# Kernel optimization log

Hardware: AMD Instinct MI355X
Metric: run time of the kernel (lower is better)

Reference implementation:

```python
import jax, jax.numpy as jnp
import numpy as np

# VoxelGrid constants (create_empty not shown in source; fixed to a realistic dense grid)
W, L, H = 64, 64, 64
VOXEL_SIZE = 0.05
ORIGIN = 0.0  # per-axis origin, same for all batches
ROUNDING_OFFSET = 0.5
MIN_POINTS_PER_VOXEL = 10


def setup_inputs() -> dict:
    key = jax.random.key(0)
    k1, k2 = jax.random.split(key)
    B, C, N = 4, 32, 200_000
    extent = W * VOXEL_SIZE  # 3.2
    # uniform coords slightly extending past the grid so a few points are OOB
    point_coordinates = jax.random.uniform(
        k1, (B, 3, N), jnp.float32, minval=-0.02, maxval=extent + 0.02)
    point_attributes = jax.random.normal(k2, (B, C, N), jnp.float32)
    return {"point_coordinates": point_coordinates,
            "point_attributes": point_attributes}


def reference(point_coordinates, point_attributes):
    B, C, N = point_attributes.shape
    V = W * L * H
    bounds = jnp.array([W, L, H], jnp.int32)

    # point -> integer voxel coordinates (origin = 0)
    coords = jnp.floor((point_coordinates - ORIGIN) / VOXEL_SIZE
                       + ROUNDING_OFFSET).astype(jnp.int32)      # [B,3,N]
    in_bounds = jnp.all((coords >= 0) & (coords < bounds[None, :, None]),
                        axis=1)                                   # [B,N]
    flat = coords[:, 0] * (L * H) + coords[:, 1] * H + coords[:, 2]
    # route OOB points to segment V which is dropped by segment ops
    flat = jnp.where(in_bounds, flat, V)                          # [B,N]

    def per_batch(idx, attrs, mask):
        # idx [N] int32, attrs [C,N], mask [N] bool
        counts = jax.ops.segment_sum(mask.astype(jnp.int32), idx,
                                     num_segments=V)              # [V]
        vals = jnp.where(mask[None, :], attrs, -jnp.inf)          # [C,N]
        pooled = jax.ops.segment_max(vals.T, idx, num_segments=V).T  # [C,V]
        pooled = jnp.where(counts[None, :] > 0, pooled, jnp.zeros_like(pooled))
        occ = (counts >= MIN_POINTS_PER_VOXEL).astype(attrs.dtype)   # [V]
        return pooled, occ

    data, occ = jax.vmap(per_batch)(flat, point_attributes, in_bounds)
    voxeldata = data.reshape(B, C, W, L, H)
    voxeloccupancy = occ.reshape(B, 1, W, L, H)
    return voxeldata, voxeloccupancy
```

## Files before the change

### kernel.cpp

```cpp
#include <hip/hip_runtime.h>
#include <math.h>


#define GW 64
#define GL 64
#define GH 64
#define GV (GW * GL * GH)
#define NB 4
#define MIN_PTS 10

__device__ __forceinline__ int bin_coord(float x) {
    float m = __fmul_rn(x, 20.0f);
    float r = __fadd_rn(m, 0.5f);
    return (int)floorf(r);
}

__global__ void zero_kernel(uint4* __restrict__ p, int n4) {
    int i = blockIdx.x * blockDim.x + threadIdx.x;
    if (i < n4) p[i] = make_uint4(0u, 0u, 0u, 0u);
}

__global__ void hist_transpose_kernel(const float* __restrict__ coords,
                                      const float* __restrict__ attrs,
                                      int* __restrict__ counts,
                                      int* __restrict__ vox,
                                      int* __restrict__ rank,
                                      float* __restrict__ attrsT,
                                      size_t strideT,
                                      int b0, int N) {
    __shared__ float lds[4][64 * 33];
    int t = threadIdx.x;
    int w = t >> 6;
    int l = t & 63;
    int n = blockIdx.x * 256 + t;
    int b = b0 + blockIdx.y;

    if (n < N) {
        const float* pc = coords + (size_t)b * 3 * N;
        int ix = bin_coord(pc[n]);
        int iy = bin_coord(pc[n + N]);
        int iz = bin_coord(pc[n + 2 * N]);
        bool ok = (unsigned)ix < (unsigned)GW && (unsigned)iy < (unsigned)GL &&
                  (unsigned)iz < (unsigned)GH;
        int v = ok ? ((ix << 12) | (iy << 6) | iz) : -1;
        vox[(size_t)b * N + n] = v;
        if (ok) rank[(size_t)b * N + n] = atomicAdd(&counts[b * GV + v], 1);

        const float* pa = attrs + (size_t)b * 32 * N + n;
        float* row = &lds[w][l * 33];
#pragma unroll
        for (int c = 0; c < 32; ++c)
            row[c] = pa[(size_t)c * N];
    }
    __syncthreads();

    float* dbase = attrsT + (size_t)blockIdx.y * strideT;
    int wbase = blockIdx.x * 256 + w * 64;
    int j = l & 7;
#pragma unroll
    for (int s = 0; s < 8; ++s) {
        int q = s * 8 + (l >> 3);
        int p = wbase + q;
        if (p < N) {
            const float* src = &lds[w][q * 33 + j * 4];
            float4 val = make_float4(src[0], src[1], src[2], src[3]);
            *(float4*)&dbase[(size_t)p * 32 + j * 4] = val;
        }
    }
}

__global__ void hist_kernel(const float* __restrict__ coords,
                            int* __restrict__ counts,
                            int* __restrict__ vox,
                            int* __restrict__ rank,
                            int N) {
    int n = blockIdx.x * blockDim.x + threadIdx.x;
    int b = blockIdx.y;
    if (n >= N) return;
    const float* pc = coords + (size_t)b * 3 * N;
    int ix = bin_coord(pc[n]);
    int iy = bin_coord(pc[n + N]);
    int iz = bin_coord(pc[n + 2 * N]);
    bool ok = (unsigned)ix < (unsigned)GW && (unsigned)iy < (unsigned)GL &&
              (unsigned)iz < (unsigned)GH;
    int v = ok ? ((ix << 12) | (iy << 6) | iz) : -1;
    vox[(size_t)b * N + n] = v;
    if (ok) rank[(size_t)b * N + n] = atomicAdd(&counts[b * GV + v], 1);
}

__global__ void transpose_kernel(const float* __restrict__ attrs,
                                 float* __restrict__ attrsT,
                                 size_t strideT, int b0, int N) {
    __shared__ float lds[4][64 * 33];
    int t = threadIdx.x;
    int w = t >> 6;
    int l = t & 63;
    int n = blockIdx.x * 256 + t;
    int b = b0 + blockIdx.y;
    if (n < N) {
        const float* pa = attrs + (size_t)b * 32 * N + n;
        float* row = &lds[w][l * 33];
#pragma unroll
        for (int c = 0; c < 32; ++c)
            row[c] = pa[(size_t)c * N];
    }
    __syncthreads();
    float* dbase = attrsT + (size_t)blockIdx.y * strideT;
    int wbase = blockIdx.x * 256 + w * 64;
    int j = l & 7;
#pragma unroll
    for (int s = 0; s < 8; ++s) {
        int q = s * 8 + (l >> 3);
        int p = wbase + q;
        if (p < N) {
            const float* src = &lds[w][q * 33 + j * 4];
            float4 val = make_float4(src[0], src[1], src[2], src[3]);
            *(float4*)&dbase[(size_t)p * 32 + j * 4] = val;
        }
    }
}

__global__ void scan_blocks_kernel(const int* __restrict__ counts,
                                   int* __restrict__ offsets,
                                   int* __restrict__ blocksums) {
    __shared__ int lds[256];
    int t = threadIdx.x;
    int base = blockIdx.x * 1024 + t * 4;
    int4 c = *(const int4*)&counts[base];
    int s0 = c.x, s1 = s0 + c.y, s2 = s1 + c.z, s3 = s2 + c.w;
    lds[t] = s3;
    __syncthreads();
    for (int d = 1; d < 256; d <<= 1) {
        int v = (t >= d) ? lds[t - d] : 0;
        __syncthreads();
        if (t >= d) lds[t] += v;
        __syncthreads();
    }
    int excl = (t > 0) ? lds[t - 1] : 0;
    int4 o;
    o.x = excl; o.y = excl + s0; o.z = excl + s1; o.w = excl + s2;
    *(int4*)&offsets[base] = o;
    if (t == 255) blocksums[blockIdx.x] = lds[255];
}

__global__ void scan_sums_kernel(int* __restrict__ blocksums) {
    __shared__ int lds[256];
    int t = threadIdx.x;
    int4 c = *(const int4*)&blocksums[t * 4];
    int s0 = c.x, s1 = s0 + c.y, s2 = s1 + c.z, s3 = s2 + c.w;
    lds[t] = s3;
    __syncthreads();
    for (int d = 1; d < 256; d <<= 1) {
        int v = (t >= d) ? lds[t - d] : 0;
        __syncthreads();
        if (t >= d) lds[t] += v;
        __syncthreads();
    }
    int excl = (t > 0) ? lds[t - 1] : 0;
    int4 o;
    o.x = excl; o.y = excl + s0; o.z = excl + s1; o.w = excl + s2;
    *(int4*)&blocksums[t * 4] = o;
}

__global__ void scan_add_kernel(int* __restrict__ offsets,
                                const int* __restrict__ blocksums) {
    int i = blockIdx.x * blockDim.x + threadIdx.x;
    int s = blocksums[(i * 4) >> 10];
    int4 o = *(int4*)&offsets[i * 4];
    o.x += s; o.y += s; o.z += s; o.w += s;
    *(int4*)&offsets[i * 4] = o;
}

__global__ void scatter_idx_kernel(const int* __restrict__ vox,
                                   const int* __restrict__ rank,
                                   const int* __restrict__ offsets,
                                   int* __restrict__ sorted_idx,
                                   int N) {
    int n = blockIdx.x * blockDim.x + threadIdx.x;
    int b = blockIdx.y;
    if (n >= N) return;
    int v = vox[(size_t)b * N + n];
    if (v < 0) return;
    sorted_idx[offsets[b * GV + v] + rank[(size_t)b * N + n]] = n;
}

__global__ void segmax3_kernel(const float* __restrict__ attrsT,
                               const int* __restrict__ counts,
                               const int* __restrict__ offsets,
                               const int* __restrict__ sorted_idx,
                               float* __restrict__ vdata,
                               float* __restrict__ occ,
                               size_t strideT,
                               int b0) {
    __shared__ float acc[64 * 33];
    __shared__ int cnt_l[64];
    __shared__ int off_l[64];
    int t = threadIdx.x;
    int w = t >> 6;
    int lane = t & 63;
    int g = lane >> 5;
    int c = lane & 31;
    int b = b0 + blockIdx.y;
    int v0 = blockIdx.x * 64;

    if (t < 64) {
        int bv = b * GV + v0 + t;
        cnt_l[t] = counts[bv];
        off_l[t] = offsets[bv];
    }
    __syncthreads();

    const float* sbase = attrsT + (size_t)blockIdx.y * strideT;
#pragma unroll
    for (int pp = 0; pp < 8; ++pp) {
        int vl = w * 16 + pp * 2 + g;
        int cnt = cnt_l[vl];
        int off = off_l[vl];
        float m = -INFINITY;
        for (int k = 0; k < cnt; ++k) {
            int idx = sorted_idx[off + k];
            m = fmaxf(m, sbase[(size_t)idx * 32 + c]);
        }
        acc[vl * 33 + c] = (cnt > 0) ? m : 0.0f;
    }
    __syncthreads();

    int vv = v0 + lane;
#pragma unroll
    for (int cc = 0; cc < 8; ++cc) {
        int ch = cc * 4 + w;
        vdata[(((size_t)(b * 32 + ch)) << 18) + vv] = acc[lane * 33 + ch];
    }
    if (t < 64)
        occ[b * GV + v0 + t] = (cnt_l[t] >= MIN_PTS) ? 1.0f : 0.0f;
}

__global__ void segmax_kernel(const float* __restrict__ attrs,
                              const int* __restrict__ counts,
                              const int* __restrict__ offsets,
                              const int* __restrict__ sorted_idx,
                              float* __restrict__ vdata,
                              float* __restrict__ occ,
                              int N) {
    int t = blockIdx.x * blockDim.x + threadIdx.x;
    int v = t & (GV - 1);
    int c = (t >> 18) & 31;
    int b = t >> 23;
    int bv = (b << 18) | v;
    int cnt = counts[bv];
    int off = offsets[bv];
    const float* row = attrs + ((size_t)(b * 32 + c)) * N;
    float m = -INFINITY;
    for (int k = 0; k < cnt; ++k) {
        m = fmaxf(m, row[sorted_idx[off + k]]);
    }
    vdata[((size_t)(b * 32 + c) << 18) | v] = (cnt > 0) ? m : 0.0f;
    if (c == 0) occ[bv] = (cnt >= MIN_PTS) ? 1.0f : 0.0f;
}

__device__ __forceinline__ unsigned enc_f32(float f) {
    unsigned u = __float_as_uint(f);
    return (u & 0x80000000u) ? ~u : (u | 0x80000000u);
}
__device__ __forceinline__ float dec_f32(unsigned u) {
    return (u & 0x80000000u) ? __uint_as_float(u & 0x7FFFFFFFu)
                             : __uint_as_float(~u);
}

__global__ void init_kernel(uint4* __restrict__ data4, uint4* __restrict__ cnt4,
                            int nData4, int nCnt4) {
    int i = blockIdx.x * blockDim.x + threadIdx.x;
    uint4 z = make_uint4(0u, 0u, 0u, 0u);
    if (i < nData4) data4[i] = z;
    else if (i < nData4 + nCnt4) cnt4[i - nData4] = z;
}

__global__ void scatter_kernel(const float* __restrict__ coords,
                               const float* __restrict__ attrs,
                               unsigned* __restrict__ bits,
                               int* __restrict__ counts,
                               int N, int C) {
    int n = blockIdx.x * blockDim.x + threadIdx.x;
    int b = blockIdx.y;
    if (n >= N) return;
    const float* pc = coords + (size_t)b * 3 * N;
    int ix = bin_coord(pc[n]);
    int iy = bin_coord(pc[n + N]);
    int iz = bin_coord(pc[n + 2 * N]);
    if ((unsigned)ix >= (unsigned)GW || (unsigned)iy >= (unsigned)GL ||
        (unsigned)iz >= (unsigned)GH)
        return;
    int v = (ix << 12) | (iy << 6) | iz;
    atomicAdd(&counts[b * GV + v], 1);
    const float* pa = attrs + (size_t)b * C * N + n;
    unsigned* pb = bits + (size_t)b * C * GV + v;
    for (int c = 0; c < C; ++c)
        atomicMax(&pb[(size_t)c * GV], enc_f32(pa[(size_t)c * N]));
}

__global__ void finalize_kernel(unsigned* __restrict__ data,
                                const int* __restrict__ counts,
                                float* __restrict__ occ, int C) {
    int i = blockIdx.x * blockDim.x + threadIdx.x;
    int nData4 = NB * C * GV / 4;
    int nOcc4 = NB * GV / 4;
    if (i < nData4) {
        int idx = i << 2;
        int v = idx & (GV - 1);
        int b = idx / (C * GV);
        int4 cv = *(const int4*)&counts[b * GV + v];
        uint4 u = *(const uint4*)&data[idx];
        float4 r;
        r.x = cv.x > 0 ? dec_f32(u.x) : 0.0f;
        r.y = cv.y > 0 ? dec_f32(u.y) : 0.0f;
        r.z = cv.z > 0 ? dec_f32(u.z) : 0.0f;
        r.w = cv.w > 0 ? dec_f32(u.w) : 0.0f;
        *(float4*)&data[idx] = r;
    } else if (i < nData4 + nOcc4) {
        int j = (i - nData4) << 2;
        int4 cv = *(const int4*)&counts[j];
        float4 r;
        r.x = cv.x >= MIN_PTS ? 1.0f : 0.0f;
        r.y = cv.y >= MIN_PTS ? 1.0f : 0.0f;
        r.z = cv.z >= MIN_PTS ? 1.0f : 0.0f;
        r.w = cv.w >= MIN_PTS ? 1.0f : 0.0f;
        *(float4*)&occ[j] = r;
    }
}

extern "C" void kernel_launch(void* const* d_in, const int* in_sizes, int n_in,
                              void* d_out, int out_size, void* d_ws, size_t ws_size,
                              hipStream_t stream) {
    const float* coords = (const float*)d_in[0];
    const float* attrs  = (const float*)d_in[1];
    int N = in_sizes[0] / (NB * 3);
    int C = in_sizes[1] / (NB * N);

    size_t wsCommon = (size_t)(2 * NB * GV + 4096 + 3 * NB * N) * 4;
    size_t oneT  = (size_t)N * 32 * 4;
    size_t fullT = (size_t)NB * N * 32 * 4;

    if (C == 32 && ws_size >= wsCommon + oneT) {
        int* counts     = (int*)d_ws;
        int* offsets    = counts + (size_t)NB * GV;
        int* blocksums  = offsets + (size_t)NB * GV;
        int* vox        = blocksums + 4096;
        int* rank       = vox + (size_t)NB * N;
        int* sorted_idx = rank + (size_t)NB * N;
        float* attrsT   = (float*)(sorted_idx + (size_t)NB * N);
        float* vdata    = (float*)d_out;
        float* occ      = (float*)d_out + (size_t)NB * 32 * GV;

        int nCnt4 = NB * GV / 4;
        zero_kernel<<<(nCnt4 + 255) / 256, 256, 0, stream>>>((uint4*)counts,
                                                             nCnt4);
        dim3 pgrid((N + 255) / 256, NB);
        bool full = (ws_size >= wsCommon + fullT);

        if (full) {
            hist_transpose_kernel<<<pgrid, 256, 0, stream>>>(
                coords, attrs, counts, vox, rank, attrsT, (size_t)N * 32, 0, N);
        } else {
            hist_kernel<<<pgrid, 256, 0, stream>>>(coords, counts, vox, rank,
                                                   N);
        }

        scan_blocks_kernel<<<NB * GV / 1024, 256, 0, stream>>>(counts, offsets,
                                                               blocksums);
        scan_sums_kernel<<<1, 256, 0, stream>>>(blocksums);
        scan_add_kernel<<<NB * GV / 1024, 256, 0, stream>>>(offsets, blocksums);

        scatter_idx_kernel<<<pgrid, 256, 0, stream>>>(vox, rank, offsets,
                                                      sorted_idx, N);

        if (full) {
            segmax3_kernel<<<dim3(GV / 64, NB), 256, 0, stream>>>(
                attrsT, counts, offsets, sorted_idx, vdata, occ,
                (size_t)N * 32, 0);
        } else {
            for (int b = 0; b < NB; ++b) {
                transpose_kernel<<<dim3((N + 255) / 256, 1), 256, 0, stream>>>(
                    attrs, attrsT, 0, b, N);
                segmax3_kernel<<<dim3(GV / 64, 1), 256, 0, stream>>>(
                    attrsT, counts, offsets, sorted_idx, vdata, occ, 0, b);
            }
        }
    } else if (C == 32 &&
               ws_size >= (size_t)(2 * NB * GV + 4096 + 3 * NB * N) * 4) {
        int* counts     = (int*)d_ws;
        int* offsets    = counts + (size_t)NB * GV;
        int* blocksums  = offsets + (size_t)NB * GV;
        int* vox        = blocksums + 4096;
        int* rank       = vox + (size_t)NB * N;
        int* sorted_idx = rank + (size_t)NB * N;
        float* vdata    = (float*)d_out;
        float* occ      = (float*)d_out + (size_t)NB * 32 * GV;

        int nCnt4 = NB * GV / 4;
        zero_kernel<<<(nCnt4 + 255) / 256, 256, 0, stream>>>((uint4*)counts,
                                                             nCnt4);
        dim3 pgrid((N + 255) / 256, NB);
        hist_kernel<<<pgrid, 256, 0, stream>>>(coords, counts, vox, rank, N);

        scan_blocks_kernel<<<NB * GV / 1024, 256, 0, stream>>>(counts, offsets,
                                                               blocksums);
        scan_sums_kernel<<<1, 256, 0, stream>>>(blocksums);
        scan_add_kernel<<<NB * GV / 1024, 256, 0, stream>>>(offsets, blocksums);

        scatter_idx_kernel<<<pgrid, 256, 0, stream>>>(vox, rank, offsets,
                                                      sorted_idx, N);

        int segThreads = NB * 32 * GV;
        segmax_kernel<<<segThreads / 256, 256, 0, stream>>>(
            attrs, counts, offsets, sorted_idx, vdata, occ, N);
    } else {
        unsigned* bits = (unsigned*)d_out;
        float* occ = (float*)d_out + (size_t)NB * C * GV;
        int* counts = (int*)d_ws;
        int nData4 = NB * C * GV / 4;
        int nCnt4 = NB * GV / 4;
        int initTotal = nData4 + nCnt4;
        init_kernel<<<(initTotal + 255) / 256, 256, 0, stream>>>(
            (uint4*)d_out, (uint4*)d_ws, nData4, nCnt4);
        dim3 sgrid((N + 255) / 256, NB);
        scatter_kernel<<<sgrid, 256, 0, stream>>>(coords, attrs, bits, counts,
                                                  N, C);
        finalize_kernel<<<(initTotal + 255) / 256, 256, 0, stream>>>(
            bits, counts, occ, C);
    }
}
```

Baseline: 324.0 us.

## Stage sorted indices in LDS and vectorize segment-max reads as float4

The segment-max kernel now loads each block's contiguous range of sorted point indices into shared memory in chunks of 512. Each thread then handles two voxels and reads four channels per point with float4 loads, where before it read one channel per voxel across eight voxel passes. This is meant to cut redundant global reads of sorted_idx and the number of load instructions. In exchange it adds extra block-wide syncs per chunk and some load imbalance when voxel counts differ.

```diff
diff --git a/kernel.cpp b/kernel.cpp
--- a/kernel.cpp
+++ b/kernel.cpp
@@ -184,7 +184,7 @@
     sorted_idx[offsets[b * GV + v] + rank[(size_t)b * N + n]] = n;
 }
 
-__global__ void segmax3_kernel(const float* __restrict__ attrsT,
+__global__ void segmax4_kernel(const float* __restrict__ attrsT,
                                const int* __restrict__ counts,
                                const int* __restrict__ offsets,
                                const int* __restrict__ sorted_idx,
@@ -195,11 +195,12 @@
     __shared__ float acc[64 * 33];
     __shared__ int cnt_l[64];
     __shared__ int off_l[64];
+    __shared__ int sidx[512];
     int t = threadIdx.x;
     int w = t >> 6;
-    int lane = t & 63;
-    int g = lane >> 5;
-    int c = lane & 31;
+    int l = t & 63;
+    int vo = l >> 3;
+    int j = l & 7;
     int b = b0 + blockIdx.y;
     int v0 = blockIdx.x * 64;
 
@@ -209,27 +210,58 @@
         off_l[t] = offsets[bv];
     }
     __syncthreads();
-
+    int off0 = off_l[0];
+    int npts = off_l[63] + cnt_l[63] - off0;
+
+    int vl0 = w * 16 + vo;
+    int vl1 = w * 16 + 8 + vo;
+    int ks0 = off_l[vl0] - off0, ke0 = ks0 + cnt_l[vl0];
+    int ks1 = off_l[vl1] - off0, ke1 = ks1 + cnt_l[vl1];
+
+    float4 m0 = make_float4(-INFINITY, -INFINITY, -INFINITY, -INFINITY);
+    float4 m1 = m0;
     const float* sbase = attrsT + (size_t)blockIdx.y * strideT;
-#pragma unroll
-    for (int pp = 0; pp < 8; ++pp) {
-        int vl = w * 16 + pp * 2 + g;
-        int cnt = cnt_l[vl];
-        int off = off_l[vl];
-        float m = -INFINITY;
-        for (int k = 0; k < cnt; ++k) {
-            int idx = sorted_idx[off + k];
-            m = fmaxf(m, sbase[(size_t)idx * 32 + c]);
-        }
-        acc[vl * 33 + c] = (cnt > 0) ? m : 0.0f;
-    }
-    __syncthreads();
-
-    int vv = v0 + lane;
+    const int* sgl = sorted_idx + off0;
+
+    for (int base = 0; base < npts; base += 512) {
+        __syncthreads();
+        int mm = npts - base; if (mm > 512) mm = 512;
+        for (int i = t; i < mm; i += 256) sidx[i] = sgl[base + i];
+        __syncthreads();
+        int hi = base + mm;
+        int lo0 = ks0 > base ? ks0 : base, h0 = ke0 < hi ? ke0 : hi;
+        for (int k = lo0; k < h0; ++k) {
+            int idx = sidx[k - base];
+            float4 x = *(const float4*)&sbase[(size_t)idx * 32 + j * 4];
+            m0.x = fmaxf(m0.x, x.x); m0.y = fmaxf(m0.y, x.y);
+            m0.z = fmaxf(m0.z, x.z); m0.w = fmaxf(m0.w, x.w);
+        }
+        int lo1 = ks1 > base ? ks1 : base, h1 = ke1 < hi ? ke1 : hi;
+        for (int k = lo1; k < h1; ++k) {
+            int idx = sidx[k - base];
+            float4 x = *(const float4*)&sbase[(size_t)idx * 32 + j * 4];
+            m1.x = fmaxf(m1.x, x.x); m1.y = fmaxf(m1.y, x.y);
+            m1.z = fmaxf(m1.z, x.z); m1.w = fmaxf(m1.w, x.w);
+        }
+    }
+
+    int c4 = j * 4;
+    bool nz0 = cnt_l[vl0] > 0, nz1 = cnt_l[vl1] > 0;
+    acc[vl0 * 33 + c4 + 0] = nz0 ? m0.x : 0.0f;
+    acc[vl0 * 33 + c4 + 1] = nz0 ? m0.y : 0.0f;
+    acc[vl0 * 33 + c4 + 2] = nz0 ? m0.z : 0.0f;
+    acc[vl0 * 33 + c4 + 3] = nz0 ? m0.w : 0.0f;
+    acc[vl1 * 33 + c4 + 0] = nz1 ? m1.x : 0.0f;
+    acc[vl1 * 33 + c4 + 1] = nz1 ? m1.y : 0.0f;
+    acc[vl1 * 33 + c4 + 2] = nz1 ? m1.z : 0.0f;
+    acc[vl1 * 33 + c4 + 3] = nz1 ? m1.w : 0.0f;
+    __syncthreads();
+
+    int vv = v0 + l;
 #pragma unroll
     for (int cc = 0; cc < 8; ++cc) {
         int ch = cc * 4 + w;
-        vdata[(((size_t)(b * 32 + ch)) << 18) + vv] = acc[lane * 33 + ch];
+        vdata[(((size_t)(b * 32 + ch)) << 18) + vv] = acc[l * 33 + ch];
     }
     if (t < 64)
         occ[b * GV + v0 + t] = (cnt_l[t] >= MIN_PTS) ? 1.0f : 0.0f;
@@ -374,14 +406,14 @@
                                                       sorted_idx, N);
 
         if (full) {
-            segmax3_kernel<<<dim3(GV / 64, NB), 256, 0, stream>>>(
+            segmax4_kernel<<<dim3(GV / 64, NB), 256, 0, stream>>>(
                 attrsT, counts, offsets, sorted_idx, vdata, occ,
                 (size_t)N * 32, 0);
         } else {
             for (int b = 0; b < NB; ++b) {
                 transpose_kernel<<<dim3((N + 255) / 256, 1), 256, 0, stream>>>(
                     attrs, attrsT, 0, b, N);
-                segmax3_kernel<<<dim3(GV / 64, 1), 256, 0, stream>>>(
+                segmax4_kernel<<<dim3(GV / 64, 1), 256, 0, stream>>>(
                     attrsT, counts, offsets, sorted_idx, vdata, occ, 0, b);
             }
         }
```

After: 300.5 us. 7.2% less time.
